# Kernel optimization log

Measured on AMD Instinct MI355X. Metric: run time of the kernel, lower is better.

Reference implementation:

```python
import jax, jax.numpy as jnp
import numpy as np

N, C, H, W = 4, 128, 128, 128
G, K, PAD, DIL = 4, 3, 1, 1
P = K * K
HID = 4 * C
EPS = 1e-6


def ln(x, w, b):
    m = jnp.mean(x, -1, keepdims=True)
    v = jnp.mean((x - m) ** 2, -1, keepdims=True)
    return (x - m) * jax.lax.rsqrt(v + EPS) * w + b


def linear(x, w, b):
    return x @ w.T + b


def grid_sample_zeros(img, grid):
    # img: (B,Hi,Wi,Cc); grid: (B,L,P,2) xy in [-1,1]; bilinear, zeros padding, align_corners=False
    B, Hi, Wi, Cc = img.shape
    gx = (grid[..., 0] + 1.0) * (Wi * 0.5) - 0.5
    gy = (grid[..., 1] + 1.0) * (Hi * 0.5) - 0.5
    x0 = jnp.floor(gx)
    y0 = jnp.floor(gy)
    wx1 = gx - x0
    wy1 = gy - y0
    flat = img.reshape(B, Hi * Wi, Cc)
    Bq, L, Pq = gx.shape

    def tap(yy, xx, wgt):
        valid = (xx >= 0) & (xx <= Wi - 1) & (yy >= 0) & (yy <= Hi - 1)
        idx = (jnp.clip(yy, 0, Hi - 1) * Wi + jnp.clip(xx, 0, Wi - 1)).astype(jnp.int32)
        v = jnp.take_along_axis(flat, idx.reshape(B, L * Pq)[..., None], axis=1)
        return v.reshape(B, L, Pq, Cc) * (wgt * valid)[..., None]

    return (tap(y0, x0, (1 - wx1) * (1 - wy1))
            + tap(y0, x0 + 1, wx1 * (1 - wy1))
            + tap(y0 + 1, x0, (1 - wx1) * wy1)
            + tap(y0 + 1, x0 + 1, wx1 * wy1))


def dcn_core(x, offset, mask):
    # faithful port of dcnv3_core_pytorch (stride=1, offset_scale=1.0)
    n, h, w, c = x.shape
    gc = c // G
    xp = jnp.pad(x, ((0, 0), (PAD, PAD), (PAD, PAD), (0, 0)))
    hi, wi = h + 2 * PAD, w + 2 * PAD
    base = (DIL * (K - 1)) // 2 + 0.5
    ref_y = (base + jnp.arange(h, dtype=jnp.float32)) / hi
    ref_x = (base + jnp.arange(w, dtype=jnp.float32)) / wi
    ref = jnp.stack([jnp.broadcast_to(ref_x[None, :], (h, w)),
                     jnp.broadcast_to(ref_y[:, None], (h, w))], -1)  # (h,w,2) xy
    ks = jnp.arange(K, dtype=jnp.float32) * DIL - (DIL * (K - 1)) // 2
    gxk, gyk = jnp.meshgrid(ks, ks, indexing='ij')  # x slow, y fast (torch meshgrid order)
    grid = jnp.tile(jnp.stack([gxk / wi, gyk / hi], -1).reshape(P, 2), (G, 1))  # (G*P,2)
    sn = jnp.array([wi, hi], jnp.float32)
    loc = ref[None, :, :, None, :] + grid[None, None, None] + offset.reshape(n, h, w, G * P, 2) / sn
    sg = (2.0 * loc - 1.0).reshape(n, h * w, G, P, 2).transpose(0, 2, 1, 3, 4).reshape(n * G, h * w, P, 2)
    img = xp.reshape(n, hi, wi, G, gc).transpose(0, 3, 1, 2, 4).reshape(n * G, hi, wi, gc)
    samp = grid_sample_zeros(img, sg)  # (n*G, h*w, P, gc)
    m = mask.reshape(n, h * w, G, P).transpose(0, 2, 1, 3).reshape(n * G, h * w, P)
    out = jnp.einsum('blpc,blp->blc', samp, m)
    return out.reshape(n, G, h * w, gc).transpose(0, 2, 1, 3).reshape(n, h, w, c)


def dcn_forward(xcl, dw_w, dw_b, dwln_w, dwln_b, off_w, off_b, mask_w, mask_b, outproj_w, outproj_b):
    n, h, w, c = xcl.shape
    y = jax.lax.conv_general_dilated(xcl.transpose(0, 3, 1, 2), dw_w, (1, 1),
                                     ((PAD, PAD), (PAD, PAD)),
                                     dimension_numbers=('NCHW', 'OIHW', 'NCHW'),
                                     feature_group_count=C)
    y = y + dw_b[None, :, None, None]
    x1 = jax.nn.gelu(ln(y.transpose(0, 2, 3, 1), dwln_w, dwln_b), approximate=False)
    offset = linear(x1, off_w, off_b)
    m = jax.nn.softmax(linear(x1, mask_w, mask_b).reshape(n, h, w, G, P), -1).reshape(n, h, w, G * P)
    out = dcn_core(x1, offset, m)
    return linear(out, outproj_w, outproj_b)


def setup_inputs():
    key = jax.random.key(0)
    ks = jax.random.split(key, 8)
    s = 0.02
    return {
        "x": jax.random.normal(ks[0], (N, C, H, W), jnp.float32),
        "norm1_w": jnp.ones((C,), jnp.float32), "norm1_b": jnp.zeros((C,), jnp.float32),
        "dw_w": jax.random.normal(ks[1], (C, 1, K, K), jnp.float32) * 0.1,
        "dw_b": jnp.zeros((C,), jnp.float32),
        "dwln_w": jnp.ones((C,), jnp.float32), "dwln_b": jnp.zeros((C,), jnp.float32),
        "off_w": jax.random.normal(ks[2], (G * P * 2, C), jnp.float32) * 0.05,
        "off_b": jax.random.normal(ks[3], (G * P * 2,), jnp.float32) * 0.5,
        "mask_w": jax.random.normal(ks[4], (G * P, C), jnp.float32) * 0.05,
        "mask_b": jnp.zeros((G * P,), jnp.float32),
        "outproj_w": jax.random.normal(ks[5], (C, C), jnp.float32) * s,
        "outproj_b": jnp.zeros((C,), jnp.float32),
        "norm2_w": jnp.ones((C,), jnp.float32), "norm2_b": jnp.zeros((C,), jnp.float32),
        "fc1_w": jax.random.normal(ks[6], (HID, C), jnp.float32) * s,
        "fc1_b": jnp.zeros((HID,), jnp.float32),
        "fc2_w": jax.random.normal(ks[7], (C, HID), jnp.float32) * s,
        "fc2_b": jnp.zeros((C,), jnp.float32),
    }


def reference(x, norm1_w, norm1_b, dw_w, dw_b, dwln_w, dwln_b, off_w, off_b,
              mask_w, mask_b, outproj_w, outproj_b, norm2_w, norm2_b,
              fc1_w, fc1_b, fc2_w, fc2_b):
    # pre-norm branch (layer_scale=None, post_norm=False, res_post_norm=False, drop_path=Identity)
    xcl = ln(x.transpose(0, 2, 3, 1), norm1_w, norm1_b)  # channels_first -> channels_last LN
    d = dcn_forward(xcl, dw_w, dw_b, dwln_w, dwln_b, off_w, off_b, mask_w, mask_b, outproj_w, outproj_b)
    x = x + d.transpose(0, 3, 1, 2)
    y = ln(x.transpose(0, 2, 3, 1), norm2_w, norm2_b)
    y = linear(jax.nn.gelu(linear(y, fc1_w, fc1_b), approximate=False), fc2_w, fc2_b)
    return x + y.transpose(0, 3, 1, 2)
```

## Files before the change

### kernel.cpp

```cpp
#include <hip/hip_runtime.h>

typedef unsigned short ushort_t;
typedef short short8 __attribute__((ext_vector_type(8)));
typedef float f32x4 __attribute__((ext_vector_type(4)));
typedef ushort_t ushort8v __attribute__((ext_vector_type(8)));
typedef ushort_t ushort4v __attribute__((ext_vector_type(4)));

#define HWsz 16384
#define NHWsz 65536
#define YS 136
#define HS 520

__device__ __forceinline__ float b2f(ushort_t u){ return __uint_as_float(((unsigned)u)<<16); }
__device__ __forceinline__ ushort_t f2b(float f){
  unsigned x = __float_as_uint(f);
  x += 0x7fffu + ((x>>16)&1u);
  return (ushort_t)(x>>16);
}
__device__ __forceinline__ float gelu_fast(float x){
  float t = x*x;
  float e = __expf(x*(1.5957691216f + 0.0713548163f*t));
  return x - x*__builtin_amdgcn_rcpf(1.0f + e);
}

__global__ __launch_bounds__(256) void kW_cvt(const float* __restrict__ w1, const float* __restrict__ w2,
    const float* __restrict__ offw, const float* __restrict__ maskw, const float* __restrict__ dww,
    const float* __restrict__ pw, const float* __restrict__ offb, const float* __restrict__ mb,
    ushort_t* __restrict__ w1b, ushort_t* __restrict__ w2b, ushort_t* __restrict__ owmb,
    float* __restrict__ dwwT, ushort_t* __restrict__ pwh, ushort_t* __restrict__ pwl,
    float* __restrict__ obm){
  int i = blockIdx.x*256 + threadIdx.x;
  w1b[i] = f2b(w1[i]);
  w2b[i] = f2b(w2[i]);
  if (i < 16384){
    int row = i >> 7, k = i & 127;
    float v = 0.f;
    if (row < 72) v = offw[row*128 + k];
    else if (row < 108) v = maskw[(row-72)*128 + k];
    owmb[i] = f2b(v);
    float pv = pw[i];
    ushort_t hi = f2b(pv);
    pwh[i] = hi;
    pwl[i] = f2b(pv - b2f(hi));
  }
  if (i < 1152){
    int k = i >> 7, c = i & 127;
    dwwT[i] = dww[c*9 + k];
  }
  if (i < 128){
    obm[i] = (i < 72) ? offb[i] : ((i < 108) ? mb[i-72] : 0.f);
  }
}

__global__ __launch_bounds__(256) void kA_ln1(const float* __restrict__ x,
    const float* __restrict__ w, const float* __restrict__ b,
    ushort_t* __restrict__ xcl){
  __shared__ float tile[128*66];
  __shared__ float psum[256], psq[256];
  __shared__ float ms[64], rs[64];
  int t = threadIdx.x;
  int pos0 = blockIdx.x * 64;
  int n = pos0 >> 14, hw0 = pos0 & 16383;
  const float* xb = x + (size_t)n*128*HWsz + hw0;
  for (int i=0;i<32;i++){
    int e = i*256+t;
    int c = e>>6, p = e&63;
    tile[c*66+p] = xb[(size_t)c*HWsz + p];
  }
  __syncthreads();
  {
    int part = t>>6, p = t&63;
    float s=0.f, q=0.f;
    for (int c=part*32; c<part*32+32; c++){ float v = tile[c*66+p]; s+=v; q+=v*v; }
    psum[part*64+p]=s; psq[part*64+p]=q;
  }
  __syncthreads();
  if (t<64){
    float s=psum[t]+psum[64+t]+psum[128+t]+psum[192+t];
    float q=psq[t]+psq[64+t]+psq[128+t]+psq[192+t];
    float m = s*(1.0f/128.0f);
    float v = q*(1.0f/128.0f)-m*m;
    ms[t]=m; rs[t]=rsqrtf(v+1e-6f);
  }
  __syncthreads();
  for (int i=0;i<32;i++){
    int e = i*256+t;
    int p = e>>7, c = e&127;
    float v = (tile[c*66+p]-ms[p])*rs[p]*w[c]+b[c];
    xcl[(size_t)(pos0+p)*128 + c] = f2b(v);
  }
}

__global__ __launch_bounds__(256) void kB_dw(const ushort_t* __restrict__ xcl,
    const float* __restrict__ dwwT, const float* __restrict__ dwb,
    const float* __restrict__ lnw, const float* __restrict__ lnb,
    ushort_t* __restrict__ x1){
  __shared__ float partS[16*17], partQ[16*17];
  __shared__ float ms[16], rs[16];
  int t = threadIdx.x;
  int pos0 = blockIdx.x*16;
  int n = pos0>>14, hw0 = pos0&16383, h = hw0>>7, w0 = hw0&127;
  int pp = t>>4, l = t&15, ch0 = l*8;
  int w = w0 + pp;
  float acc[8];
  {
    float4 b0 = *(const float4*)(dwb + ch0);
    float4 b1 = *(const float4*)(dwb + ch0 + 4);
    acc[0]=b0.x; acc[1]=b0.y; acc[2]=b0.z; acc[3]=b0.w;
    acc[4]=b1.x; acc[5]=b1.y; acc[6]=b1.z; acc[7]=b1.w;
  }
  #pragma unroll
  for (int kh=0; kh<3; kh++){
    int hy = h + kh - 1;
    if ((unsigned)hy < 128u){
      #pragma unroll
      for (int kw=0; kw<3; kw++){
        int wx = w + kw - 1;
        if ((unsigned)wx < 128u){
          ushort8v xv = *(const ushort8v*)(xcl + ((size_t)(n*16384 + hy*128 + wx))*128 + ch0);
          const float* wr = dwwT + (kh*3+kw)*128 + ch0;
          float4 w0v = *(const float4*)(wr);
          float4 w1v = *(const float4*)(wr+4);
          acc[0] += b2f(xv[0])*w0v.x; acc[1] += b2f(xv[1])*w0v.y;
          acc[2] += b2f(xv[2])*w0v.z; acc[3] += b2f(xv[3])*w0v.w;
          acc[4] += b2f(xv[4])*w1v.x; acc[5] += b2f(xv[5])*w1v.y;
          acc[6] += b2f(xv[6])*w1v.z; acc[7] += b2f(xv[7])*w1v.w;
        }
      }
    }
  }
  {
    float s=0.f, q=0.f;
    #pragma unroll
    for (int j=0;j<8;j++){ s+=acc[j]; q+=acc[j]*acc[j]; }
    partS[pp*17+l]=s; partQ[pp*17+l]=q;
  }
  __syncthreads();
  if (t<16){
    float s=0.f, q=0.f;
    for (int i=0;i<16;i++){ s += partS[t*17+i]; q += partQ[t*17+i]; }
    float m = s*(1.0f/128.0f);
    float var = q*(1.0f/128.0f) - m*m;
    ms[t]=m; rs[t]=rsqrtf(var+1e-6f);
  }
  __syncthreads();
  {
    float m = ms[pp], r = rs[pp];
    float4 lw0 = *(const float4*)(lnw + ch0);
    float4 lw1 = *(const float4*)(lnw + ch0 + 4);
    float4 lb0 = *(const float4*)(lnb + ch0);
    float4 lb1 = *(const float4*)(lnb + ch0 + 4);
    float lw[8] = {lw0.x,lw0.y,lw0.z,lw0.w,lw1.x,lw1.y,lw1.z,lw1.w};
    float lb[8] = {lb0.x,lb0.y,lb0.z,lb0.w,lb1.x,lb1.y,lb1.z,lb1.w};
    ushort8v o;
    #pragma unroll
    for (int j=0;j<8;j++){
      float v = (acc[j]-m)*r*lw[j]+lb[j];
      o[j] = f2b(gelu_fast(v));
    }
    *(ushort8v*)(x1 + (size_t)(pos0+pp)*128 + ch0) = o;
  }
}

#define RS 120
__global__ __launch_bounds__(256) void kCD_dcn(const ushort_t* __restrict__ x1,
    const ushort_t* __restrict__ owmb, const float* __restrict__ obm,
    ushort_t* __restrict__ dcnout){
  __shared__ __align__(16) ushort_t xLb[16*YS];
  __shared__ float raw[16*RS];
  __shared__ __align__(16) float descW[576*4];
  __shared__ __align__(16) int   descO[576*4];
  int t = threadIdx.x;
  int pos0 = blockIdx.x*16;
  int n = pos0>>14, hw0 = pos0&16383, h = hw0>>7, w0 = hw0&127;
  const size_t imgbase = (size_t)n*16384*128;

  *(ushort8v*)(xLb + (t>>4)*YS + (t&15)*8) = *(const ushort8v*)(x1 + (size_t)pos0*128 + t*8);
  __syncthreads();

  {
    int wave = t>>6, lane = t&63;
    int ma = lane&15, quad = lane>>4;
    short8 afrag[4];
    #pragma unroll
    for (int ks=0; ks<4; ks++)
      afrag[ks] = *(const short8*)(xLb + ma*YS + ks*32 + quad*8);
    f32x4 acc[2];
    acc[0] = (f32x4){0.f,0.f,0.f,0.f};
    acc[1] = (f32x4){0.f,0.f,0.f,0.f};
    #pragma unroll
    for (int tile=0; tile<2; tile++){
      const ushort_t* brow = owmb + (size_t)(wave*32 + tile*16 + ma)*128 + quad*8;
      #pragma unroll
      for (int ks=0; ks<4; ks++){
        short8 bfrag = *(const short8*)(brow + ks*32);
        acc[tile] = __builtin_amdgcn_mfma_f32_16x16x32_bf16(bfrag, afrag[ks], acc[tile], 0,0,0);
      }
    }
    #pragma unroll
    for (int tile=0; tile<2; tile++){
      int row0 = wave*32 + tile*16 + quad*4;
      if (row0 < 112){
        f32x4 bias4 = *(const f32x4*)(obm + row0);
        f32x4 o;
        #pragma unroll
        for (int r=0;r<4;r++) o[r] = acc[tile][r] + bias4[r];
        *(f32x4*)(raw + ma*RS + row0) = o;
      }
    }
  }
  __syncthreads();

  if (t < 64){
    int p = t>>2, g = t&3;
    float* mr = raw + p*RS + 72 + g*9;
    float mx = -1e30f;
    for (int q=0;q<9;q++) mx = fmaxf(mx, mr[q]);
    float e[9]; float ssum=0.f;
    for (int q=0;q<9;q++){ e[q]=expf(mr[q]-mx); ssum+=e[q]; }
    float inv = 1.0f/ssum;
    for (int q=0;q<9;q++) mr[q] = e[q]*inv;
  }
  __syncthreads();

  for (int it=0; it<3; it++){
    int tid = t + 256*it;
    if (tid < 576){
      int pp = tid/36, rem = tid - pp*36;
      int g = rem/9, p = rem - g*9;
      int i = p/3, j = p - i*3;
      float ox = raw[pp*RS + 2*(g*9+p)];
      float oy = raw[pp*RS + 2*(g*9+p)+1];
      float mval = raw[pp*RS + 72 + g*9 + p];
      float px = (float)(w0 + pp + i - 1) + ox;
      float py = (float)(h + j - 1) + oy;
      float fx0 = floorf(px), fy0 = floorf(py);
      int ix0 = (int)fx0, iy0 = (int)fy0;
      float fx = px - fx0, fy = py - fy0;
      float vx0 = ((unsigned)ix0     < 128u) ? 1.f : 0.f;
      float vx1 = ((unsigned)(ix0+1) < 128u) ? 1.f : 0.f;
      float vy0 = ((unsigned)iy0     < 128u) ? 1.f : 0.f;
      float vy1 = ((unsigned)(iy0+1) < 128u) ? 1.f : 0.f;
      int cx0 = min(max(ix0,0),127), cx1 = min(max(ix0+1,0),127);
      int cy0 = min(max(iy0,0),127), cy1 = min(max(iy0+1,0),127);
      float4 wv;
      wv.x = (1.f-fx)*(1.f-fy)*mval*vx0*vy0;
      wv.y = fx*(1.f-fy)*mval*vx1*vy0;
      wv.z = (1.f-fx)*fy*mval*vx0*vy1;
      wv.w = fx*fy*mval*vx1*vy1;
      int4 ov;
      ov.x = (cy0*128+cx0)*128;
      ov.y = (cy0*128+cx1)*128;
      ov.z = (cy1*128+cx0)*128;
      ov.w = (cy1*128+cx1)*128;
      *(float4*)(descW + tid*4) = wv;
      *(int4*)(descO + tid*4) = ov;
    }
  }
  __syncthreads();

  {
    int pp = t>>4, l = t&15;
    int ch0 = l*8, g = l>>2;
    const ushort_t* ib = x1 + imgbase + ch0;
    float acc[8];
    #pragma unroll
    for (int j=0;j<8;j++) acc[j]=0.f;
    int dbase = pp*36 + g*9;
    #pragma unroll
    for (int p=0;p<9;p++){
      float4 wv = *(const float4*)(descW + (dbase+p)*4);
      int4  ov = *(const int4*)(descO + (dbase+p)*4);
      ushort8v v00 = *(const ushort8v*)(ib + ov.x);
      ushort8v v10 = *(const ushort8v*)(ib + ov.y);
      ushort8v v01 = *(const ushort8v*)(ib + ov.z);
      ushort8v v11 = *(const ushort8v*)(ib + ov.w);
      #pragma unroll
      for (int j=0;j<8;j++){
        float s = wv.x*b2f(v00[j]) + wv.y*b2f(v10[j]) + wv.z*b2f(v01[j]) + wv.w*b2f(v11[j]);
        acc[j] += s;
      }
    }
    ushort8v outv;
    #pragma unroll
    for (int j=0;j<8;j++) outv[j] = f2b(acc[j]);
    *(ushort8v*)(dcnout + (size_t)(pos0+pp)*128 + ch0) = outv;
  }
}

__global__ __launch_bounds__(256) void kE_outproj(const ushort_t* dcnout,
    const ushort_t* __restrict__ pwh, const ushort_t* __restrict__ pwl,
    const float* __restrict__ pb, const float* __restrict__ x,
    const float* __restrict__ n2w, const float* __restrict__ n2b,
    ushort_t* __restrict__ x2, ushort_t* x2n){
  __shared__ float partS[32*17], partQ[32*17];
  __shared__ float msh[32], rsh[32];
  int t = threadIdx.x;
  int pos0 = blockIdx.x*32;
  int n = pos0>>14, hw0 = pos0&16383;
  int wave = t>>6, lane = t&63;
  int ma = lane&15, quad = lane>>4;

  short8 af[2][4];
  #pragma unroll
  for (int mt=0; mt<2; mt++)
    #pragma unroll
    for (int ks=0; ks<4; ks++)
      af[mt][ks] = *(const short8*)(dcnout + (size_t)(pos0+mt*16+ma)*128 + ks*32 + quad*8);

  f32x4 acc[2][2];
  #pragma unroll
  for (int i=0;i<2;i++){ acc[i][0]=(f32x4){0.f,0.f,0.f,0.f}; acc[i][1]=(f32x4){0.f,0.f,0.f,0.f}; }
  #pragma unroll
  for (int tile=0; tile<2; tile++){
    int c0 = wave*32 + tile*16;
    const ushort_t* bh = pwh + (size_t)(c0 + ma)*128 + quad*8;
    const ushort_t* bl = pwl + (size_t)(c0 + ma)*128 + quad*8;
    #pragma unroll
    for (int ks=0; ks<4; ks++){
      short8 bfh = *(const short8*)(bh + ks*32);
      short8 bfl = *(const short8*)(bl + ks*32);
      #pragma unroll
      for (int mt=0; mt<2; mt++){
        acc[tile][mt] = __builtin_amdgcn_mfma_f32_16x16x32_bf16(bfh, af[mt][ks], acc[tile][mt], 0,0,0);
        acc[tile][mt] = __builtin_amdgcn_mfma_f32_16x16x32_bf16(bfl, af[mt][ks], acc[tile][mt], 0,0,0);
      }
    }
  }
  float vb[2][2][4];
  float sAcc[2], qAcc[2];
  sAcc[0]=0.f; sAcc[1]=0.f; qAcc[0]=0.f; qAcc[1]=0.f;
  #pragma unroll
  for (int tile=0; tile<2; tile++){
    int c0 = wave*32 + tile*16 + quad*4;
    f32x4 bias4 = *(const f32x4*)(pb + c0);
    #pragma unroll
    for (int mt=0; mt<2; mt++){
      int p = mt*16 + ma;
      ushort4v ov;
      #pragma unroll
      for (int r=0;r<4;r++){
        float res = x[((size_t)(n*128) + c0 + r)*HWsz + hw0 + p];
        float v = acc[tile][mt][r] + bias4[r] + res;
        ushort_t ub = f2b(v);
        ov[r] = ub;
        float vv = b2f(ub);
        vb[tile][mt][r] = vv;
        sAcc[mt] += vv; qAcc[mt] += vv*vv;
      }
      *(ushort4v*)(x2 + (size_t)(pos0+p)*128 + c0) = ov;
    }
  }
  #pragma unroll
  for (int mt=0; mt<2; mt++){
    int p = mt*16 + ma;
    partS[p*17 + wave*4 + quad] = sAcc[mt];
    partQ[p*17 + wave*4 + quad] = qAcc[mt];
  }
  __syncthreads();
  if (t < 32){
    float s=0.f, q=0.f;
    for (int i=0;i<16;i++){ s += partS[t*17+i]; q += partQ[t*17+i]; }
    float m = s*(1.0f/128.0f);
    float var = q*(1.0f/128.0f) - m*m;
    msh[t] = m; rsh[t] = rsqrtf(var+1e-6f);
  }
  __syncthreads();
  #pragma unroll
  for (int tile=0; tile<2; tile++){
    int c0 = wave*32 + tile*16 + quad*4;
    f32x4 w4 = *(const f32x4*)(n2w + c0);
    f32x4 b4 = *(const f32x4*)(n2b + c0);
    #pragma unroll
    for (int mt=0; mt<2; mt++){
      int p = mt*16 + ma;
      float m = msh[p], r = rsh[p];
      ushort4v nv;
      #pragma unroll
      for (int rr=0;rr<4;rr++) nv[rr] = f2b((vb[tile][mt][rr]-m)*r*w4[rr] + b4[rr]);
      *(ushort4v*)(x2n + (size_t)(pos0+p)*128 + c0) = nv;
    }
  }
}

__global__ __launch_bounds__(256) void kFG_mfma(const ushort_t* __restrict__ x2n,
    const ushort_t* __restrict__ x2,
    const ushort_t* __restrict__ w1b, const float* __restrict__ b1,
    const ushort_t* __restrict__ w2b, const float* __restrict__ b2,
    float* __restrict__ out){
  __shared__ __align__(16) ushort_t hid[32*HS];
  int t = threadIdx.x;
  int pos0 = blockIdx.x*32;
  int n = pos0>>14, hw0 = pos0&16383;
  int wave = t>>6, lane = t&63;
  int ma = lane&15, quad = lane>>4;

  short8 af[2][4];
  #pragma unroll
  for (int ks=0; ks<4; ks++)
    #pragma unroll
    for (int mt=0; mt<2; mt++)
      af[mt][ks] = *(const short8*)(x2n + (size_t)(pos0+mt*16+ma)*128 + ks*32 + quad*8);

  int nbase = wave*128;
  #pragma unroll
  for (int tile=0; tile<8; tile++){
    const ushort_t* brow = w1b + (size_t)(nbase + tile*16 + ma)*128 + quad*8;
    short8 bf[4];
    #pragma unroll
    for (int ks=0; ks<4; ks++) bf[ks] = *(const short8*)(brow + ks*32);
    f32x4 a0 = (f32x4){0.f,0.f,0.f,0.f};
    f32x4 a1 = (f32x4){0.f,0.f,0.f,0.f};
    #pragma unroll
    for (int ks=0; ks<4; ks++){
      a0 = __builtin_amdgcn_mfma_f32_16x16x32_bf16(bf[ks], af[0][ks], a0, 0,0,0);
      a1 = __builtin_amdgcn_mfma_f32_16x16x32_bf16(bf[ks], af[1][ks], a1, 0,0,0);
    }
    int n0 = nbase + tile*16 + quad*4;
    f32x4 bias4 = *(const f32x4*)(b1 + n0);
    ushort4v hv0, hv1;
    #pragma unroll
    for (int r=0;r<4;r++){
      hv0[r] = f2b(gelu_fast(a0[r] + bias4[r]));
      hv1[r] = f2b(gelu_fast(a1[r] + bias4[r]));
    }
    *(ushort4v*)(hid + ma*HS + n0) = hv0;
    *(ushort4v*)(hid + (16+ma)*HS + n0) = hv1;
  }
  __syncthreads();

  f32x4 acc2[2][2];
  acc2[0][0]=(f32x4){0.f,0.f,0.f,0.f}; acc2[0][1]=(f32x4){0.f,0.f,0.f,0.f};
  acc2[1][0]=(f32x4){0.f,0.f,0.f,0.f}; acc2[1][1]=(f32x4){0.f,0.f,0.f,0.f};
  const ushort_t* hb0 = hid + ma*HS + quad*8;
  const ushort_t* hb1 = hid + (16+ma)*HS + quad*8;
  const ushort_t* wb0 = w2b + (size_t)(wave*32 + ma)*512 + quad*8;
  const ushort_t* wb1 = w2b + (size_t)(wave*32 + 16 + ma)*512 + quad*8;
  short8 hf0 = *(const short8*)(hb0);
  short8 hf1 = *(const short8*)(hb1);
  short8 bf0 = *(const short8*)(wb0);
  short8 bf1 = *(const short8*)(wb1);
  for (int ks=0; ks<15; ks++){
    short8 nhf0 = *(const short8*)(hb0 + (ks+1)*32);
    short8 nhf1 = *(const short8*)(hb1 + (ks+1)*32);
    short8 nbf0 = *(const short8*)(wb0 + (ks+1)*32);
    short8 nbf1 = *(const short8*)(wb1 + (ks+1)*32);
    acc2[0][0] = __builtin_amdgcn_mfma_f32_16x16x32_bf16(bf0, hf0, acc2[0][0], 0,0,0);
    acc2[0][1] = __builtin_amdgcn_mfma_f32_16x16x32_bf16(bf0, hf1, acc2[0][1], 0,0,0);
    acc2[1][0] = __builtin_amdgcn_mfma_f32_16x16x32_bf16(bf1, hf0, acc2[1][0], 0,0,0);
    acc2[1][1] = __builtin_amdgcn_mfma_f32_16x16x32_bf16(bf1, hf1, acc2[1][1], 0,0,0);
    hf0=nhf0; hf1=nhf1; bf0=nbf0; bf1=nbf1;
  }
  acc2[0][0] = __builtin_amdgcn_mfma_f32_16x16x32_bf16(bf0, hf0, acc2[0][0], 0,0,0);
  acc2[0][1] = __builtin_amdgcn_mfma_f32_16x16x32_bf16(bf0, hf1, acc2[0][1], 0,0,0);
  acc2[1][0] = __builtin_amdgcn_mfma_f32_16x16x32_bf16(bf1, hf0, acc2[1][0], 0,0,0);
  acc2[1][1] = __builtin_amdgcn_mfma_f32_16x16x32_bf16(bf1, hf1, acc2[1][1], 0,0,0);

  #pragma unroll
  for (int tile=0; tile<2; tile++){
    int c0 = wave*32 + tile*16 + quad*4;
    f32x4 bias4 = *(const f32x4*)(b2 + c0);
    #pragma unroll
    for (int mt=0; mt<2; mt++){
      int p = mt*16 + ma;
      ushort4v rv = *(const ushort4v*)(x2 + (size_t)(pos0+p)*128 + c0);
      #pragma unroll
      for (int r=0;r<4;r++){
        float v = acc2[tile][mt][r] + bias4[r] + b2f(rv[r]);
        out[((size_t)(n*128) + c0 + r)*HWsz + hw0 + p] = v;
      }
    }
  }
}

extern "C" void kernel_launch(void* const* d_in, const int* in_sizes, int n_in,
                              void* d_out, int out_size, void* d_ws, size_t ws_size,
                              hipStream_t stream){
  const float* x     = (const float*)d_in[0];
  const float* n1w   = (const float*)d_in[1];
  const float* n1b   = (const float*)d_in[2];
  const float* dww   = (const float*)d_in[3];
  const float* dwb   = (const float*)d_in[4];
  const float* dwlnw = (const float*)d_in[5];
  const float* dwlnb = (const float*)d_in[6];
  const float* offw  = (const float*)d_in[7];
  const float* offb  = (const float*)d_in[8];
  const float* maskw = (const float*)d_in[9];
  const float* maskb = (const float*)d_in[10];
  const float* pw    = (const float*)d_in[11];
  const float* pb    = (const float*)d_in[12];
  const float* n2w   = (const float*)d_in[13];
  const float* n2b   = (const float*)d_in[14];
  const float* w1    = (const float*)d_in[15];
  const float* b1    = (const float*)d_in[16];
  const float* w2    = (const float*)d_in[17];
  const float* b2    = (const float*)d_in[18];

  char* wsb = (char*)d_ws;
  ushort_t* R0   = (ushort_t*)(wsb);
  ushort_t* R1   = (ushort_t*)(wsb + (16u<<20));
  ushort_t* w1b  = (ushort_t*)(wsb + (32u<<20));
  ushort_t* w2b  = (ushort_t*)(wsb + (32u<<20) + (128u<<10));
  ushort_t* owmb = (ushort_t*)(wsb + (32u<<20) + (256u<<10));
  ushort_t* pwh  = (ushort_t*)(wsb + (32u<<20) + (288u<<10));
  ushort_t* pwl  = (ushort_t*)(wsb + (32u<<20) + (320u<<10));
  float*    dwwT = (float*)(wsb + (32u<<20) + (352u<<10));
  float*    obm  = (float*)(wsb + (32u<<20) + (358u<<10));
  float* out = (float*)d_out;

  hipLaunchKernelGGL(kW_cvt,  dim3(256),   dim3(256), 0, stream, w1, w2, offw, maskw, dww, pw, offb, maskb, w1b, w2b, owmb, dwwT, pwh, pwl, obm);
  hipLaunchKernelGGL(kA_ln1,  dim3(1024),  dim3(256), 0, stream, x, n1w, n1b, R0);
  hipLaunchKernelGGL(kB_dw,   dim3(4096),  dim3(256), 0, stream, R0, dwwT, dwb, dwlnw, dwlnb, R1);
  hipLaunchKernelGGL(kCD_dcn, dim3(4096),  dim3(256), 0, stream, R1, owmb, obm, R0);
  hipLaunchKernelGGL(kE_outproj, dim3(2048), dim3(256), 0, stream, R0, pwh, pwl, pb, x, n2w, n2b, R1, R0);
  hipLaunchKernelGGL(kFG_mfma, dim3(2048), dim3(256), 0, stream, R0, R1, w1b, b1, w2b, b2, out);
}
```

Before: 298.8 us.

## Fuse outproj+LN2 into MLP kernel with swizzled LDS and weight prefetch

```diff
diff --git a/kernel.cpp b/kernel.cpp
--- a/kernel.cpp
+++ b/kernel.cpp
@@ -9,7 +9,6 @@
 #define HWsz 16384
 #define NHWsz 65536
 #define YS 136
-#define HS 520
 
 __device__ __forceinline__ float b2f(ushort_t u){ return __uint_as_float(((unsigned)u)<<16); }
 __device__ __forceinline__ ushort_t f2b(float f){
@@ -22,6 +21,9 @@
   float e = __expf(x*(1.5957691216f + 0.0713548163f*t));
   return x - x*__builtin_amdgcn_rcpf(1.0f + e);
 }
+
+#define HSW(p, b) ((p)*1024 + ((b) ^ (((p)&7)<<4)))
+#define XSW(p, b) ((p)*256  + ((b) ^ (((p)&7)<<4)))
 
 __global__ __launch_bounds__(256) void kW_cvt(const float* __restrict__ w1, const float* __restrict__ w2,
     const float* __restrict__ offw, const float* __restrict__ maskw, const float* __restrict__ dww,
@@ -288,13 +290,20 @@
   }
 }
 
-__global__ __launch_bounds__(256) void kE_outproj(const ushort_t* dcnout,
+__global__ __launch_bounds__(256, 4) void kEFG(const ushort_t* __restrict__ dcnout,
     const ushort_t* __restrict__ pwh, const ushort_t* __restrict__ pwl,
     const float* __restrict__ pb, const float* __restrict__ x,
     const float* __restrict__ n2w, const float* __restrict__ n2b,
-    ushort_t* __restrict__ x2, ushort_t* x2n){
-  __shared__ float partS[32*17], partQ[32*17];
-  __shared__ float msh[32], rsh[32];
+    const ushort_t* __restrict__ w1b, const float* __restrict__ b1,
+    const ushort_t* __restrict__ w2b, const float* __restrict__ b2,
+    float* __restrict__ out){
+  __shared__ __align__(16) char hidb[32*1024];
+  __shared__ __align__(16) char xnb[32*256];
+  float* partS = (float*)hidb;
+  float* partQ = partS + 32*17;
+  float* msh   = partQ + 32*17;
+  float* rsh   = msh + 32;
+
   int t = threadIdx.x;
   int pos0 = blockIdx.x*32;
   int n = pos0>>14, hw0 = pos0&16383;
@@ -327,6 +336,7 @@
       }
     }
   }
+
   float vb[2][2][4];
   float sAcc[2], qAcc[2];
   sAcc[0]=0.f; sAcc[1]=0.f; qAcc[0]=0.f; qAcc[1]=0.f;
@@ -337,18 +347,14 @@
     #pragma unroll
     for (int mt=0; mt<2; mt++){
       int p = mt*16 + ma;
-      ushort4v ov;
       #pragma unroll
       for (int r=0;r<4;r++){
         float res = x[((size_t)(n*128) + c0 + r)*HWsz + hw0 + p];
         float v = acc[tile][mt][r] + bias4[r] + res;
-        ushort_t ub = f2b(v);
-        ov[r] = ub;
-        float vv = b2f(ub);
+        float vv = b2f(f2b(v));
         vb[tile][mt][r] = vv;
         sAcc[mt] += vv; qAcc[mt] += vv*vv;
       }
-      *(ushort4v*)(x2 + (size_t)(pos0+p)*128 + c0) = ov;
     }
   }
   #pragma unroll
@@ -366,6 +372,7 @@
     msh[t] = m; rsh[t] = rsqrtf(var+1e-6f);
   }
   __syncthreads();
+
   #pragma unroll
   for (int tile=0; tile<2; tile++){
     int c0 = wave*32 + tile*16 + quad*4;
@@ -378,43 +385,38 @@
       ushort4v nv;
       #pragma unroll
       for (int rr=0;rr<4;rr++) nv[rr] = f2b((vb[tile][mt][rr]-m)*r*w4[rr] + b4[rr]);
-      *(ushort4v*)(x2n + (size_t)(pos0+p)*128 + c0) = nv;
-    }
-  }
-}
-
-__global__ __launch_bounds__(256) void kFG_mfma(const ushort_t* __restrict__ x2n,
-    const ushort_t* __restrict__ x2,
-    const ushort_t* __restrict__ w1b, const float* __restrict__ b1,
-    const ushort_t* __restrict__ w2b, const float* __restrict__ b2,
-    float* __restrict__ out){
-  __shared__ __align__(16) ushort_t hid[32*HS];
-  int t = threadIdx.x;
-  int pos0 = blockIdx.x*32;
-  int n = pos0>>14, hw0 = pos0&16383;
-  int wave = t>>6, lane = t&63;
-  int ma = lane&15, quad = lane>>4;
-
-  short8 af[2][4];
+      *(ushort4v*)(xnb + XSW(p, c0*2)) = nv;
+    }
+  }
+  __syncthreads();
+
+  short8 axf[2][4];
   #pragma unroll
   for (int ks=0; ks<4; ks++)
     #pragma unroll
     for (int mt=0; mt<2; mt++)
-      af[mt][ks] = *(const short8*)(x2n + (size_t)(pos0+mt*16+ma)*128 + ks*32 + quad*8);
+      axf[mt][ks] = *(const short8*)(xnb + XSW(mt*16+ma, ks*64 + quad*16));
 
   int nbase = wave*128;
+  short8 wcur[4], wnxt[4];
+  {
+    const ushort_t* brow = w1b + (size_t)(nbase + ma)*128 + quad*8;
+    #pragma unroll
+    for (int ks=0; ks<4; ks++) wcur[ks] = *(const short8*)(brow + ks*32);
+  }
   #pragma unroll
   for (int tile=0; tile<8; tile++){
-    const ushort_t* brow = w1b + (size_t)(nbase + tile*16 + ma)*128 + quad*8;
-    short8 bf[4];
-    #pragma unroll
-    for (int ks=0; ks<4; ks++) bf[ks] = *(const short8*)(brow + ks*32);
+    if (tile < 7){
+      const ushort_t* brow = w1b + (size_t)(nbase + (tile+1)*16 + ma)*128 + quad*8;
+      #pragma unroll
+      for (int ks=0; ks<4; ks++) wnxt[ks] = *(const short8*)(brow + ks*32);
+    }
     f32x4 a0 = (f32x4){0.f,0.f,0.f,0.f};
     f32x4 a1 = (f32x4){0.f,0.f,0.f,0.f};
     #pragma unroll
     for (int ks=0; ks<4; ks++){
-      a0 = __builtin_amdgcn_mfma_f32_16x16x32_bf16(bf[ks], af[0][ks], a0, 0,0,0);
-      a1 = __builtin_amdgcn_mfma_f32_16x16x32_bf16(bf[ks], af[1][ks], a1, 0,0,0);
+      a0 = __builtin_amdgcn_mfma_f32_16x16x32_bf16(wcur[ks], axf[0][ks], a0, 0,0,0);
+      a1 = __builtin_amdgcn_mfma_f32_16x16x32_bf16(wcur[ks], axf[1][ks], a1, 0,0,0);
     }
     int n0 = nbase + tile*16 + quad*4;
     f32x4 bias4 = *(const f32x4*)(b1 + n0);
@@ -424,37 +426,37 @@
       hv0[r] = f2b(gelu_fast(a0[r] + bias4[r]));
       hv1[r] = f2b(gelu_fast(a1[r] + bias4[r]));
     }
-    *(ushort4v*)(hid + ma*HS + n0) = hv0;
-    *(ushort4v*)(hid + (16+ma)*HS + n0) = hv1;
+    *(ushort4v*)(hidb + HSW(ma,    n0*2)) = hv0;
+    *(ushort4v*)(hidb + HSW(16+ma, n0*2)) = hv1;
+    #pragma unroll
+    for (int ks=0; ks<4; ks++) wcur[ks] = wnxt[ks];
   }
   __syncthreads();
 
   f32x4 acc2[2][2];
   acc2[0][0]=(f32x4){0.f,0.f,0.f,0.f}; acc2[0][1]=(f32x4){0.f,0.f,0.f,0.f};
   acc2[1][0]=(f32x4){0.f,0.f,0.f,0.f}; acc2[1][1]=(f32x4){0.f,0.f,0.f,0.f};
-  const ushort_t* hb0 = hid + ma*HS + quad*8;
-  const ushort_t* hb1 = hid + (16+ma)*HS + quad*8;
   const ushort_t* wb0 = w2b + (size_t)(wave*32 + ma)*512 + quad*8;
   const ushort_t* wb1 = w2b + (size_t)(wave*32 + 16 + ma)*512 + quad*8;
-  short8 hf0 = *(const short8*)(hb0);
-  short8 hf1 = *(const short8*)(hb1);
-  short8 bf0 = *(const short8*)(wb0);
-  short8 bf1 = *(const short8*)(wb1);
-  for (int ks=0; ks<15; ks++){
-    short8 nhf0 = *(const short8*)(hb0 + (ks+1)*32);
-    short8 nhf1 = *(const short8*)(hb1 + (ks+1)*32);
-    short8 nbf0 = *(const short8*)(wb0 + (ks+1)*32);
-    short8 nbf1 = *(const short8*)(wb1 + (ks+1)*32);
-    acc2[0][0] = __builtin_amdgcn_mfma_f32_16x16x32_bf16(bf0, hf0, acc2[0][0], 0,0,0);
-    acc2[0][1] = __builtin_amdgcn_mfma_f32_16x16x32_bf16(bf0, hf1, acc2[0][1], 0,0,0);
-    acc2[1][0] = __builtin_amdgcn_mfma_f32_16x16x32_bf16(bf1, hf0, acc2[1][0], 0,0,0);
-    acc2[1][1] = __builtin_amdgcn_mfma_f32_16x16x32_bf16(bf1, hf1, acc2[1][1], 0,0,0);
-    hf0=nhf0; hf1=nhf1; bf0=nbf0; bf1=nbf1;
-  }
-  acc2[0][0] = __builtin_amdgcn_mfma_f32_16x16x32_bf16(bf0, hf0, acc2[0][0], 0,0,0);
-  acc2[0][1] = __builtin_amdgcn_mfma_f32_16x16x32_bf16(bf0, hf1, acc2[0][1], 0,0,0);
-  acc2[1][0] = __builtin_amdgcn_mfma_f32_16x16x32_bf16(bf1, hf0, acc2[1][0], 0,0,0);
-  acc2[1][1] = __builtin_amdgcn_mfma_f32_16x16x32_bf16(bf1, hf1, acc2[1][1], 0,0,0);
+  short8 hc0 = *(const short8*)(hidb + HSW(ma,    quad*16));
+  short8 hc1 = *(const short8*)(hidb + HSW(16+ma, quad*16));
+  short8 wc0 = *(const short8*)(wb0);
+  short8 wc1 = *(const short8*)(wb1);
+  #pragma unroll
+  for (int ks=0; ks<16; ks++){
+    short8 hn0, hn1, wn0, wn1;
+    if (ks < 15){
+      hn0 = *(const short8*)(hidb + HSW(ma,    (ks+1)*64 + quad*16));
+      hn1 = *(const short8*)(hidb + HSW(16+ma, (ks+1)*64 + quad*16));
+      wn0 = *(const short8*)(wb0 + (ks+1)*32);
+      wn1 = *(const short8*)(wb1 + (ks+1)*32);
+    }
+    acc2[0][0] = __builtin_amdgcn_mfma_f32_16x16x32_bf16(wc0, hc0, acc2[0][0], 0,0,0);
+    acc2[0][1] = __builtin_amdgcn_mfma_f32_16x16x32_bf16(wc0, hc1, acc2[0][1], 0,0,0);
+    acc2[1][0] = __builtin_amdgcn_mfma_f32_16x16x32_bf16(wc1, hc0, acc2[1][0], 0,0,0);
+    acc2[1][1] = __builtin_amdgcn_mfma_f32_16x16x32_bf16(wc1, hc1, acc2[1][1], 0,0,0);
+    if (ks < 15){ hc0=hn0; hc1=hn1; wc0=wn0; wc1=wn1; }
+  }
 
   #pragma unroll
   for (int tile=0; tile<2; tile++){
@@ -463,10 +465,9 @@
     #pragma unroll
     for (int mt=0; mt<2; mt++){
       int p = mt*16 + ma;
-      ushort4v rv = *(const ushort4v*)(x2 + (size_t)(pos0+p)*128 + c0);
       #pragma unroll
       for (int r=0;r<4;r++){
-        float v = acc2[tile][mt][r] + bias4[r] + b2f(rv[r]);
+        float v = acc2[tile][mt][r] + bias4[r] + vb[tile][mt][r];
         out[((size_t)(n*128) + c0 + r)*HWsz + hw0 + p] = v;
       }
     }
@@ -512,6 +513,5 @@
   hipLaunchKernelGGL(kA_ln1,  dim3(1024),  dim3(256), 0, stream, x, n1w, n1b, R0);
   hipLaunchKernelGGL(kB_dw,   dim3(4096),  dim3(256), 0, stream, R0, dwwT, dwb, dwlnw, dwlnb, R1);
   hipLaunchKernelGGL(kCD_dcn, dim3(4096),  dim3(256), 0, stream, R1, owmb, obm, R0);
-  hipLaunchKernelGGL(kE_outproj, dim3(2048), dim3(256), 0, stream, R0, pwh, pwl, pb, x, n2w, n2b, R1, R0);
-  hipLaunchKernelGGL(kFG_mfma, dim3(2048), dim3(256), 0, stream, R0, R1, w1b, b1, w2b, b2, out);
-}
+  hipLaunchKernelGGL(kEFG,    dim3(2048),  dim3(256), 0, stream, R0, pwh, pwl, pb, x, n2w, n2b, w1b, b1, w2b, b2, out);
+}
```

New measurement: 276.9 us. 1.08x faster.
